# Kernel tuning notes

Measured on AMD Instinct MI355X. Metric: run time of the kernel, lower is better.

Reference implementation:

```python
import jax, jax.numpy as jnp
import numpy as np

N, C, W = 16, 512, 4096          # batch lines, channels, max width (frames)
FINAL_DIM = 512
MASK_WIDTH = 4
NUM_NEGATIVES = 10
NUM_MASKS = 256                  # ~ mask_prob * T_total / mask_width


def _build_static():
    # Deterministic ragged lengths, already descending (pack_padded_sequence order).
    seq_len = (W - 128 * np.arange(N)).astype(np.int64)       # [4096, 3968, ..., 2176]
    t = np.arange(W)[:, None]                                  # time-major outer axis
    b = np.arange(N)[None, :]
    valid = seq_len[None, :] > t                               # [W, N]
    # pack_padded_sequence layout: for each t, all batches with len>t (desc length order)
    pack_idx = ((b * W + t)[valid]).astype(np.int64)           # [T_total] indices into flat (N*W)
    T = pack_idx.shape[0]                                      # 50176
    n_blocks = T // MASK_WIDTH
    rng = np.random.default_rng(0)
    perm = rng.permutation(n_blocks)
    sel1 = np.sort(perm[:NUM_MASKS])
    sel2 = np.sort(perm[NUM_MASKS:NUM_MASKS + NUM_NEGATIVES * NUM_MASKS])
    off = np.arange(MASK_WIDTH)
    # non-overlapping contiguous mask_width blocks, ascending (boolean-mask gather order)
    masked_idx = (sel1[:, None] * MASK_WIDTH + off).ravel().astype(np.int64)   # mask == 1
    neg_idx = (sel2[:, None] * MASK_WIDTH + off).ravel().astype(np.int64)      # mask == 2
    return seq_len, pack_idx, masked_idx, neg_idx


def setup_inputs() -> dict:
    key = jax.random.key(0)
    k1, k2, k3 = jax.random.split(key, 3)
    seq_len, pack_idx, masked_idx, neg_idx = _build_static()
    inputs = jax.random.normal(k1, (N, C, 1, W), dtype=jnp.float32)
    mask_emb = jax.random.normal(k2, (MASK_WIDTH, C), dtype=jnp.float32) * 0.02
    Wq = jax.random.normal(k3, (FINAL_DIM, C), dtype=jnp.float32) * (1.0 / np.sqrt(C))
    bq = jnp.zeros((FINAL_DIM,), dtype=jnp.float32)
    return {
        'inputs': inputs,
        'seq_len': jnp.asarray(seq_len, jnp.int32),
        'pack_idx': jnp.asarray(pack_idx, jnp.int32),
        'masked_idx': jnp.asarray(masked_idx, jnp.int32),
        'neg_idx': jnp.asarray(neg_idx, jnp.int32),
        'mask_emb': mask_emb,
        'Wq': Wq,
        'bq': bq,
    }


def reference(inputs, seq_len, pack_idx, masked_idx, neg_idx, mask_emb, Wq, bq):
    Nn, Cc, H, Ww = inputs.shape                              # H == 1
    # (N, C, 1, W) -> (N, W, 1, C) -> flat (N*W, C)
    x = jnp.transpose(inputs, (0, 3, 2, 1)).reshape(Nn * Ww, Cc)
    packed = x[pack_idx]                                      # [T_total, C] packed (time-major)
    # project_q on masked (mask==1) and negative (mask==2) token groups
    unmasked = (packed[masked_idx] @ Wq.T + bq).reshape(1, NUM_MASKS, MASK_WIDTH, FINAL_DIM)
    negatives = (packed[neg_idx] @ Wq.T + bq).reshape(NUM_NEGATIVES, NUM_MASKS, MASK_WIDTH, FINAL_DIM)
    # overwrite masked positions with the repeated mask embedding table
    packed = packed.at[masked_idx].set(jnp.tile(mask_emb, (NUM_MASKS, 1)))
    # pad_packed_sequence: scatter back to padded (N, W, C), zeros elsewhere
    out = jnp.zeros((Nn * Ww, Cc), dtype=inputs.dtype).at[pack_idx].set(packed)
    out = out.reshape(Nn, Ww, Cc).transpose(0, 2, 1)[:, :, None, :]   # (N, C, 1, W)
    return out, unmasked, negatives
```

## Files before the change

### kernel.cpp

```cpp
#include <hip/hip_runtime.h>

#define NB 16
#define CC 512
#define WW 4096
#define FD 512
#define NMASK 1024
#define T_COMB 11264
#define OUT0_ELEMS (NB*CC*WW)

#define WS_LOOKUP_OFF 0
#define WS_WQ_OFF     262144
#define WS_A_OFF      786432

#define S_LDS 36

typedef __attribute__((ext_vector_type(8))) short short8;
typedef __attribute__((ext_vector_type(4))) float f32x4;
typedef __attribute__((ext_vector_type(4))) unsigned short u16x4;

__device__ __forceinline__ unsigned short f2bf(float x) {
  unsigned int u = __builtin_bit_cast(unsigned int, x);
  u += 0x7fffu + ((u >> 16) & 1u);
  return (unsigned short)(u >> 16);
}

__device__ __forceinline__ void gload_lds16(const void* gp, void* lp) {
  __builtin_amdgcn_global_load_lds(
      (__attribute__((address_space(1))) void*)(gp),
      (__attribute__((address_space(3))) void*)(lp),
      16, 0, 0);
}

__global__ __launch_bounds__(256) void scatter_lookup_k(
    const int* __restrict__ pack_idx, const int* __restrict__ masked_idx,
    const int* __restrict__ neg_idx, int* __restrict__ lookup) {
  int g = blockIdx.x * 256 + threadIdx.x;
  int pidx = (g < NMASK) ? masked_idx[g] : neg_idx[g - NMASK];
  lookup[pack_idx[pidx]] = g;
}

__global__ __launch_bounds__(256) void fused_copy_k(
    const float* __restrict__ in, const int* __restrict__ seq_len,
    const int* __restrict__ lookup, const float* __restrict__ mask_emb,
    const float* __restrict__ Wq, float* __restrict__ out0,
    unsigned short* __restrict__ A_ws, unsigned short* __restrict__ Wq_ws) {
  if (blockIdx.x >= 2048) {
    int b2 = blockIdx.x - 2048;
    const f32x4* wq4 = (const f32x4*)Wq;
#pragma unroll
    for (int it = 0; it < 4; ++it) {
      int i4 = it * 16384 + b2 * 256 + (int)threadIdx.x;
      f32x4 v = wq4[i4];
      u16x4 o;
      o[0] = f2bf(v[0]); o[1] = f2bf(v[1]); o[2] = f2bf(v[2]); o[3] = f2bf(v[3]);
      ((u16x4*)Wq_ws)[i4] = o;
    }
    return;
  }
  const int tid = threadIdx.x;
  const int bx = blockIdx.x;
  const int n = bx >> 7;
  const int w0 = (bx & 127) * 32;
  const int wl4 = (tid & 7) * 4;
  const int w = w0 + wl4;
  const int c0 = tid >> 3;
  const size_t rowbase = ((size_t)n << 21) + (size_t)w;
  f32x4* out4 = (f32x4*)out0;
  const int L = seq_len[n];

  if (w0 + 32 > L) {
    f32x4 z = {0.f, 0.f, 0.f, 0.f};
#pragma unroll
    for (int it = 0; it < 16; ++it) {
      int c = it * 32 + c0;
      __builtin_nontemporal_store(z, &out4[(rowbase + ((size_t)c << 12)) >> 2]);
    }
    return;
  }

  __shared__ unsigned short tile[CC * S_LDS];
  __shared__ int g_s[32];
  if (tid < 32) g_s[tid] = lookup[n * WW + w0 + tid];

  const int4 g4 = *(const int4*)&lookup[n * WW + w];
  const int gg[4] = {g4.x, g4.y, g4.z, g4.w};
  bool lane_has_mask = ((unsigned)gg[0] < (unsigned)NMASK) |
                       ((unsigned)gg[1] < (unsigned)NMASK) |
                       ((unsigned)gg[2] < (unsigned)NMASK) |
                       ((unsigned)gg[3] < (unsigned)NMASK);
  bool lane_has_sel = (gg[0] >= 0) | (gg[1] >= 0) | (gg[2] >= 0) | (gg[3] >= 0);
  bool has_mask = __ballot(lane_has_mask) != 0ull;
  bool has_sel = __ballot(lane_has_sel) != 0ull;

  const f32x4* in4 = (const f32x4*)in;
#pragma unroll
  for (int it = 0; it < 16; ++it) {
    int c = it * 32 + c0;
    size_t i4 = (rowbase + ((size_t)c << 12)) >> 2;
    f32x4 v = __builtin_nontemporal_load(&in4[i4]);
    if (has_sel) {
      u16x4 bf;
      bf[0] = f2bf(v[0]); bf[1] = f2bf(v[1]);
      bf[2] = f2bf(v[2]); bf[3] = f2bf(v[3]);
      *(u16x4*)&tile[c * S_LDS + wl4] = bf;
    }
    if (has_mask) {
      float o[4] = {v[0], v[1], v[2], v[3]};
#pragma unroll
      for (int k = 0; k < 4; ++k)
        if ((unsigned)gg[k] < (unsigned)NMASK)
          o[k] = mask_emb[(gg[k] & 3) * CC + c];
      v[0] = o[0]; v[1] = o[1]; v[2] = o[2]; v[3] = o[3];
    }
    __builtin_nontemporal_store(v, &out4[i4]);
  }
  if (!has_sel) return;
  __syncthreads();

  const int lane = tid & 63;
  bool sel = (lane < 32) && (g_s[lane & 31] >= 0);
  unsigned smask = (unsigned)__ballot(sel);
  const int c2 = tid * 2;
  while (smask) {
    int wl = __builtin_ctz(smask);
    smask &= smask - 1;
    int g = g_s[wl];
    ushort2 val;
    val.x = tile[c2 * S_LDS + wl];
    val.y = tile[(c2 + 1) * S_LDS + wl];
    *(ushort2*)&A_ws[(size_t)g * CC + c2] = val;
  }
}

__global__ __launch_bounds__(256) void gemm_k(
    const unsigned short* __restrict__ A, const unsigned short* __restrict__ B,
    const float* __restrict__ bq, float* __restrict__ out) {
  __shared__ unsigned short As[2][64 * 64];
  __shared__ unsigned short Bs[2][128 * 64];
  const int tid = threadIdx.x;
  const int lane = tid & 63;
  const int quad = lane >> 4;
  const int r16 = lane & 15;
  const int wv = tid >> 6;
  const int id = blockIdx.x;
  const int xm = (id & 7) + ((id >> 5) << 3);
  const int yn = (id >> 3) & 3;
  const int bm = xm * 64;
  const int bf = yn * 128;
  const int wm = (wv & 1) * 32;
  const int wf = (wv >> 1) * 64;
  const int wbase = tid & ~63;

  f32x4 acc[2][4];
#pragma unroll
  for (int mi = 0; mi < 2; ++mi)
#pragma unroll
    for (int fi = 0; fi < 4; ++fi)
      acc[mi][fi] = (f32x4){0.f, 0.f, 0.f, 0.f};

#define STAGE_TILES(buf, k0)                                                  \
  do {                                                                        \
    _Pragma("unroll")                                                         \
    for (int it = 0; it < 2; ++it) {                                          \
      int ch = it * 256 + tid;                                                \
      int row = ch >> 3;                                                      \
      int l = (ch & 7) ^ (row & 7);                                           \
      gload_lds16(A + (size_t)(bm + row) * 512 + (k0) + l * 8,                \
                  &As[buf][(it * 256 + wbase) * 8]);                          \
    }                                                                         \
    _Pragma("unroll")                                                         \
    for (int it = 0; it < 4; ++it) {                                          \
      int ch = it * 256 + tid;                                                \
      int row = ch >> 3;                                                      \
      int l = (ch & 7) ^ (row & 7);                                           \
      gload_lds16(B + (size_t)(bf + row) * 512 + (k0) + l * 8,                \
                  &Bs[buf][(it * 256 + wbase) * 8]);                          \
    }                                                                         \
  } while (0)

  STAGE_TILES(0, 0);
  __syncthreads();

#pragma unroll
  for (int t = 0; t < 8; ++t) {
    const int cur = t & 1;
    if (t < 7) STAGE_TILES(cur ^ 1, (t + 1) * 64);

    short8 a[2][2], b[4][2];
#pragma unroll
    for (int mi = 0; mi < 2; ++mi) {
      int row = wm + mi * 16 + r16;
      int base = row * 64;
      int rx = (row & 7) << 3;
#pragma unroll
      for (int ks = 0; ks < 2; ++ks)
        a[mi][ks] = *(const short8*)&As[cur][base + ((((ks * 4 + quad) << 3)) ^ rx)];
    }
#pragma unroll
    for (int fi = 0; fi < 4; ++fi) {
      int row = wf + fi * 16 + r16;
      int base = row * 64;
      int rx = (row & 7) << 3;
#pragma unroll
      for (int ks = 0; ks < 2; ++ks)
        b[fi][ks] = *(const short8*)&Bs[cur][base + ((((ks * 4 + quad) << 3)) ^ rx)];
    }
#pragma unroll
    for (int ks = 0; ks < 2; ++ks)
#pragma unroll
      for (int mi = 0; mi < 2; ++mi)
#pragma unroll
        for (int fi = 0; fi < 4; ++fi)
          acc[mi][fi] = __builtin_amdgcn_mfma_f32_16x16x32_bf16(
              a[mi][ks], b[fi][ks], acc[mi][fi], 0, 0, 0);
    __syncthreads();
  }
#undef STAGE_TILES

#pragma unroll
  for (int fi = 0; fi < 4; ++fi) {
    int f = bf + wf + fi * 16 + r16;
    float bqv = bq[f];
#pragma unroll
    for (int mi = 0; mi < 2; ++mi) {
      int m0 = bm + wm + mi * 16 + quad * 4;
#pragma unroll
      for (int r = 0; r < 4; ++r)
        __builtin_nontemporal_store(acc[mi][fi][r] + bqv,
                                    &out[(size_t)(m0 + r) * 512 + f]);
    }
  }
}

extern "C" void kernel_launch(void* const* d_in, const int* in_sizes, int n_in,
                              void* d_out, int out_size, void* d_ws, size_t ws_size,
                              hipStream_t stream) {
  const float* inputs    = (const float*)d_in[0];
  const int*   seq_len   = (const int*)d_in[1];
  const int*   pack_idx  = (const int*)d_in[2];
  const int*   masked_idx= (const int*)d_in[3];
  const int*   neg_idx   = (const int*)d_in[4];
  const float* mask_emb  = (const float*)d_in[5];
  const float* Wq        = (const float*)d_in[6];
  const float* bq        = (const float*)d_in[7];
  float* out = (float*)d_out;
  char* ws = (char*)d_ws;
  int* lookup = (int*)(ws + WS_LOOKUP_OFF);
  unsigned short* wqb = (unsigned short*)(ws + WS_WQ_OFF);
  unsigned short* aws = (unsigned short*)(ws + WS_A_OFF);

  (void)hipMemsetAsync(lookup, 0xFF, NB * WW * sizeof(int), stream);
  scatter_lookup_k<<<44, 256, 0, stream>>>(pack_idx, masked_idx, neg_idx, lookup);
  fused_copy_k<<<2112, 256, 0, stream>>>(inputs, seq_len, lookup, mask_emb, Wq,
                                         out, aws, wqb);
  gemm_k<<<704, 256, 0, stream>>>(aws, wqb, bq, out + OUT0_ELEMS);
}
```

Measured before the change: 285.0 us.

## Deepen GEMM pipeline to 4-stage K=32 buffers and move Wq cast earlier

The GEMM now uses four LDS buffers of K=32 instead of two buffers of K=64. It keeps three stages in flight, using explicit vmcnt waits and raw s_barrier in place of full __syncthreads, so that global-to-LDS loads overlap MFMA work better. The Wq fp32-to-bf16 conversion blocks move from the big copy kernel into the small lookup-scatter kernel, which shortens the copy kernel's tail. The exchange is more loop iterations with less compute per barrier, and waitcnt logic that must match the number of loads issued.

```diff
diff --git a/kernel.cpp b/kernel.cpp
--- a/kernel.cpp
+++ b/kernel.cpp
@@ -31,32 +31,34 @@
       16, 0, 0);
 }
 
-__global__ __launch_bounds__(256) void scatter_lookup_k(
+__global__ __launch_bounds__(256) void scatter_wq_k(
     const int* __restrict__ pack_idx, const int* __restrict__ masked_idx,
-    const int* __restrict__ neg_idx, int* __restrict__ lookup) {
-  int g = blockIdx.x * 256 + threadIdx.x;
-  int pidx = (g < NMASK) ? masked_idx[g] : neg_idx[g - NMASK];
-  lookup[pack_idx[pidx]] = g;
+    const int* __restrict__ neg_idx, int* __restrict__ lookup,
+    const float* __restrict__ Wq, unsigned short* __restrict__ Wq_ws) {
+  const int bx = blockIdx.x;
+  const int tid = threadIdx.x;
+  if (bx < 44) {
+    int g = bx * 256 + tid;
+    int pidx = (g < NMASK) ? masked_idx[g] : neg_idx[g - NMASK];
+    lookup[pack_idx[pidx]] = g;
+    return;
+  }
+  int b2 = bx - 44;
+  const f32x4* wq4 = (const f32x4*)Wq;
+#pragma unroll
+  for (int it = 0; it < 4; ++it) {
+    int i4 = it * 16384 + b2 * 256 + tid;
+    f32x4 v = wq4[i4];
+    u16x4 o;
+    o[0] = f2bf(v[0]); o[1] = f2bf(v[1]); o[2] = f2bf(v[2]); o[3] = f2bf(v[3]);
+    ((u16x4*)Wq_ws)[i4] = o;
+  }
 }
 
 __global__ __launch_bounds__(256) void fused_copy_k(
     const float* __restrict__ in, const int* __restrict__ seq_len,
     const int* __restrict__ lookup, const float* __restrict__ mask_emb,
-    const float* __restrict__ Wq, float* __restrict__ out0,
-    unsigned short* __restrict__ A_ws, unsigned short* __restrict__ Wq_ws) {
-  if (blockIdx.x >= 2048) {
-    int b2 = blockIdx.x - 2048;
-    const f32x4* wq4 = (const f32x4*)Wq;
-#pragma unroll
-    for (int it = 0; it < 4; ++it) {
-      int i4 = it * 16384 + b2 * 256 + (int)threadIdx.x;
-      f32x4 v = wq4[i4];
-      u16x4 o;
-      o[0] = f2bf(v[0]); o[1] = f2bf(v[1]); o[2] = f2bf(v[2]); o[3] = f2bf(v[3]);
-      ((u16x4*)Wq_ws)[i4] = o;
-    }
-    return;
-  }
+    float* __restrict__ out0, unsigned short* __restrict__ A_ws) {
   const int tid = threadIdx.x;
   const int bx = blockIdx.x;
   const int n = bx >> 7;
@@ -135,8 +137,8 @@
 __global__ __launch_bounds__(256) void gemm_k(
     const unsigned short* __restrict__ A, const unsigned short* __restrict__ B,
     const float* __restrict__ bq, float* __restrict__ out) {
-  __shared__ unsigned short As[2][64 * 64];
-  __shared__ unsigned short Bs[2][128 * 64];
+  __shared__ unsigned short As[4][64 * 32];
+  __shared__ unsigned short Bs[4][128 * 32];
   const int tid = threadIdx.x;
   const int lane = tid & 63;
   const int quad = lane >> 4;
@@ -158,64 +160,62 @@
     for (int fi = 0; fi < 4; ++fi)
       acc[mi][fi] = (f32x4){0.f, 0.f, 0.f, 0.f};
 
-#define STAGE_TILES(buf, k0)                                                  \
+#define STAGE(buf, k0)                                                        \
   do {                                                                        \
+    {                                                                         \
+      int row = tid >> 2;                                                     \
+      int l = (tid & 3) ^ (row & 3);                                          \
+      gload_lds16(A + (size_t)(bm + row) * 512 + (k0) + l * 8,                \
+                  &As[buf][wbase * 8]);                                       \
+    }                                                                         \
     _Pragma("unroll")                                                         \
     for (int it = 0; it < 2; ++it) {                                          \
       int ch = it * 256 + tid;                                                \
-      int row = ch >> 3;                                                      \
-      int l = (ch & 7) ^ (row & 7);                                           \
-      gload_lds16(A + (size_t)(bm + row) * 512 + (k0) + l * 8,                \
-                  &As[buf][(it * 256 + wbase) * 8]);                          \
-    }                                                                         \
-    _Pragma("unroll")                                                         \
-    for (int it = 0; it < 4; ++it) {                                          \
-      int ch = it * 256 + tid;                                                \
-      int row = ch >> 3;                                                      \
-      int l = (ch & 7) ^ (row & 7);                                           \
+      int row = ch >> 2;                                                      \
+      int l = (ch & 3) ^ (row & 3);                                           \
       gload_lds16(B + (size_t)(bf + row) * 512 + (k0) + l * 8,                \
                   &Bs[buf][(it * 256 + wbase) * 8]);                          \
     }                                                                         \
   } while (0)
 
-  STAGE_TILES(0, 0);
-  __syncthreads();
-
-#pragma unroll
-  for (int t = 0; t < 8; ++t) {
-    const int cur = t & 1;
-    if (t < 7) STAGE_TILES(cur ^ 1, (t + 1) * 64);
-
-    short8 a[2][2], b[4][2];
+  STAGE(0, 0);
+  STAGE(1, 32);
+  STAGE(2, 64);
+  asm volatile("s_waitcnt vmcnt(6)" ::: "memory");
+  __builtin_amdgcn_s_barrier();
+
+#pragma unroll
+  for (int t = 0; t < 16; ++t) {
+    if (t < 13) STAGE((t + 3) & 3, (t + 3) * 32);
+
+    short8 a[2], b[4];
 #pragma unroll
     for (int mi = 0; mi < 2; ++mi) {
       int row = wm + mi * 16 + r16;
-      int base = row * 64;
-      int rx = (row & 7) << 3;
-#pragma unroll
-      for (int ks = 0; ks < 2; ++ks)
-        a[mi][ks] = *(const short8*)&As[cur][base + ((((ks * 4 + quad) << 3)) ^ rx)];
+      a[mi] = *(const short8*)&As[t & 3][row * 32 + ((quad ^ (row & 3)) << 3)];
     }
 #pragma unroll
     for (int fi = 0; fi < 4; ++fi) {
       int row = wf + fi * 16 + r16;
-      int base = row * 64;
-      int rx = (row & 7) << 3;
-#pragma unroll
-      for (int ks = 0; ks < 2; ++ks)
-        b[fi][ks] = *(const short8*)&Bs[cur][base + ((((ks * 4 + quad) << 3)) ^ rx)];
-    }
-#pragma unroll
-    for (int ks = 0; ks < 2; ++ks)
-#pragma unroll
-      for (int mi = 0; mi < 2; ++mi)
-#pragma unroll
-        for (int fi = 0; fi < 4; ++fi)
-          acc[mi][fi] = __builtin_amdgcn_mfma_f32_16x16x32_bf16(
-              a[mi][ks], b[fi][ks], acc[mi][fi], 0, 0, 0);
-    __syncthreads();
-  }
-#undef STAGE_TILES
+      b[fi] = *(const short8*)&Bs[t & 3][row * 32 + ((quad ^ (row & 3)) << 3)];
+    }
+#pragma unroll
+    for (int mi = 0; mi < 2; ++mi)
+#pragma unroll
+      for (int fi = 0; fi < 4; ++fi)
+        acc[mi][fi] = __builtin_amdgcn_mfma_f32_16x16x32_bf16(
+            a[mi], b[fi], acc[mi][fi], 0, 0, 0);
+
+    if (t < 13) {
+      asm volatile("s_waitcnt vmcnt(6)" ::: "memory");
+    } else if (t == 13) {
+      asm volatile("s_waitcnt vmcnt(3)" ::: "memory");
+    } else if (t == 14) {
+      asm volatile("s_waitcnt vmcnt(0)" ::: "memory");
+    }
+    if (t < 15) __builtin_amdgcn_s_barrier();
+  }
+#undef STAGE
 
 #pragma unroll
   for (int fi = 0; fi < 4; ++fi) {
@@ -250,8 +250,9 @@
   unsigned short* aws = (unsigned short*)(ws + WS_A_OFF);
 
   (void)hipMemsetAsync(lookup, 0xFF, NB * WW * sizeof(int), stream);
-  scatter_lookup_k<<<44, 256, 0, stream>>>(pack_idx, masked_idx, neg_idx, lookup);
-  fused_copy_k<<<2112, 256, 0, stream>>>(inputs, seq_len, lookup, mask_emb, Wq,
-                                         out, aws, wqb);
+  scatter_wq_k<<<108, 256, 0, stream>>>(pack_idx, masked_idx, neg_idx, lookup,
+                                        Wq, wqb);
+  fused_copy_k<<<2048, 256, 0, stream>>>(inputs, seq_len, lookup, mask_emb,
+                                         out, aws);
   gemm_k<<<704, 256, 0, stream>>>(aws, wqb, bq, out + OUT0_ELEMS);
 }
```

After: 287.3 us. No clear change (+0.8%).
